# Kernel tuning notes

Measured on AMD Instinct MI355X. Metric: run time of the kernel, lower is better.

## Reference

```python
import jax, jax.numpy as jnp
import numpy as np

N_NODES = 50000
N_EDGES = 800000
F_IN = 256
HIDDEN = 64
HEADS = 4
N_CLASS = 40
NEG_SLOPE = 0.2


def gat_layer(x, src, dst, W, al, ar, b, heads, out_dim):
    # x: [N, Fin] -> h: [N, H, D]
    N = x.shape[0]
    h = (x @ W).reshape(N, heads, out_dim)
    el = jnp.sum(h * al, axis=-1)  # [N, H]
    er = jnp.sum(h * ar, axis=-1)  # [N, H]
    e = jax.nn.leaky_relu(el[src] + er[dst], NEG_SLOPE)  # [E, H]
    # segment softmax over incoming edges of each destination node
    emax = jax.ops.segment_max(e, dst, num_segments=N)  # [N, H] (-inf for empty, unused)
    ex = jnp.exp(e - emax[dst])
    esum = jax.ops.segment_sum(ex, dst, num_segments=N)
    alpha = ex / esum[dst]  # [E, H]; esum[dst] >= ex > 0 per existing edge
    msg = h[src] * alpha[:, :, None]  # [E, H, D]
    out = jax.ops.segment_sum(msg, dst, num_segments=N)  # [N, H, D]
    return out + b.reshape(1, heads, out_dim)


def setup_inputs() -> dict:
    key = jax.random.key(0)
    ks = jax.random.split(key, 16)
    x = jax.random.normal(ks[0], (N_NODES, F_IN), dtype=jnp.float32)
    edge_index = jax.random.randint(ks[1], (2, N_EDGES), 0, N_NODES, dtype=jnp.int64)
    s = 0.1
    return {
        "x": x,
        "edge_index": edge_index,
        "W1": jax.random.normal(ks[2], (F_IN, HEADS * HIDDEN), dtype=jnp.float32) * s,
        "al1": jax.random.normal(ks[3], (HEADS, HIDDEN), dtype=jnp.float32) * s,
        "ar1": jax.random.normal(ks[4], (HEADS, HIDDEN), dtype=jnp.float32) * s,
        "b1": jnp.zeros((HEADS * HIDDEN,), dtype=jnp.float32),
        "W2": jax.random.normal(ks[5], (HEADS * HIDDEN, HEADS * HIDDEN), dtype=jnp.float32) * s,
        "al2": jax.random.normal(ks[6], (HEADS, HIDDEN), dtype=jnp.float32) * s,
        "ar2": jax.random.normal(ks[7], (HEADS, HIDDEN), dtype=jnp.float32) * s,
        "b2": jnp.zeros((HEADS * HIDDEN,), dtype=jnp.float32),
        "W3": jax.random.normal(ks[8], (HEADS * HIDDEN, N_CLASS), dtype=jnp.float32) * s,
        "al3": jax.random.normal(ks[9], (1, N_CLASS), dtype=jnp.float32) * s,
        "ar3": jax.random.normal(ks[10], (1, N_CLASS), dtype=jnp.float32) * s,
        "b3": jnp.zeros((N_CLASS,), dtype=jnp.float32),
    }


def reference(x, edge_index, W1, al1, ar1, b1, W2, al2, ar2, b2, W3, al3, ar3, b3):
    src, dst = edge_index[0], edge_index[1]
    N = x.shape[0]
    # layer 1: GATConv -> flatten heads -> ELU
    h = gat_layer(x, src, dst, W1, al1, ar1, b1, HEADS, HIDDEN).reshape(N, -1)
    h = jax.nn.elu(h)
    # layer 2
    h = gat_layer(h, src, dst, W2, al2, ar2, b2, HEADS, HIDDEN).reshape(N, -1)
    h = jax.nn.elu(h)
    # layer 3: 1 head -> mean over head dim
    h = gat_layer(h, src, dst, W3, al3, ar3, b3, 1, N_CLASS).mean(axis=1)
    return jax.nn.log_softmax(h, axis=1)
```

## Files before the change

kernel.cpp:

```cpp
#include <hip/hip_runtime.h>
#include <hip/hip_bf16.h>
#include <math.h>

#define N_NODES 50000
#define N_EDGES 800000
#define NCLASS 40
#define MAXE 512

using f32x4 = __attribute__((ext_vector_type(4))) float;
using s16x8 = __attribute__((ext_vector_type(8))) short;

__global__ void detect_i64(const int* __restrict__ raw, int* __restrict__ flag) {
  int t = threadIdx.x;
  int v = raw[2 * t + 1];
  unsigned long long any = __ballot(v != 0);
  if (t == 0) flag[0] = (any == 0ULL) ? 1 : 0;
}

__global__ void norm_count(const int* __restrict__ raw, const int* __restrict__ flag,
                           int* __restrict__ s32, int* __restrict__ d32,
                           int* __restrict__ deg) {
  int e = blockIdx.x * blockDim.x + threadIdx.x;
  if (e >= N_EDGES) return;
  int s, d;
  if (flag[0]) {
    s = raw[2 * e];
    d = raw[2 * N_EDGES + 2 * e];
  } else {
    s = raw[e];
    d = raw[N_EDGES + e];
  }
  s32[e] = s;
  d32[e] = d;
  atomicAdd(&deg[d], 1);
}

__global__ void scan_bsum(const int* __restrict__ deg, int* __restrict__ bsums) {
  __shared__ int sm[256];
  int t = threadIdx.x;
  int i = blockIdx.x * 256 + t;
  sm[t] = (i < N_NODES) ? deg[i] : 0;
  __syncthreads();
  for (int off = 128; off > 0; off >>= 1) {
    if (t < off) sm[t] += sm[t + off];
    __syncthreads();
  }
  if (t == 0) bsums[blockIdx.x] = sm[0];
}

__global__ void scan_offsets(int* __restrict__ bsums, int* __restrict__ rowp, int nb) {
  __shared__ int sm[256];
  int t = threadIdx.x;
  int v = (t < nb) ? bsums[t] : 0;
  sm[t] = v;
  __syncthreads();
  for (int off = 1; off < 256; off <<= 1) {
    int add = (t >= off) ? sm[t - off] : 0;
    __syncthreads();
    sm[t] += add;
    __syncthreads();
  }
  if (t < nb) bsums[t] = sm[t] - v;
  if (t == 0) rowp[N_NODES] = N_EDGES;
}

__global__ void scan_final(const int* __restrict__ deg, const int* __restrict__ bsums,
                           int* __restrict__ rowp, int* __restrict__ cursor) {
  __shared__ int sm[256];
  int t = threadIdx.x;
  int i = blockIdx.x * 256 + t;
  int v = (i < N_NODES) ? deg[i] : 0;
  sm[t] = v;
  __syncthreads();
  for (int off = 1; off < 256; off <<= 1) {
    int add = (t >= off) ? sm[t - off] : 0;
    __syncthreads();
    sm[t] += add;
    __syncthreads();
  }
  int excl = sm[t] - v + bsums[blockIdx.x];
  if (i < N_NODES) { rowp[i] = excl; cursor[i] = excl; }
}

__global__ void scatter_edges(const int* __restrict__ s32, const int* __restrict__ d32,
                              int* __restrict__ cursor, int* __restrict__ srcs) {
  int e = blockIdx.x * blockDim.x + threadIdx.x;
  if (e >= N_EDGES) return;
  int d = d32[e];
  int pos = atomicAdd(&cursor[d], 1);
  srcs[pos] = s32[e];
}

__global__ void tr_w(const float* __restrict__ W, __hip_bfloat16* __restrict__ WT) {
  int id = blockIdx.x * 256 + threadIdx.x;
  int n = id >> 8, k = id & 255;
  WT[n * 256 + k] = __float2bfloat16(W[k * 256 + n]);
}

__global__ void tr_w3(const float* __restrict__ W3, __hip_bfloat16* __restrict__ WT3) {
  int id = blockIdx.x * 256 + threadIdx.x;
  int n = id >> 8, k = id & 255;
  WT3[n * 256 + k] = (n < NCLASS) ? __float2bfloat16(W3[k * NCLASS + n]) : __float2bfloat16(0.f);
}

__global__ void cast_x(const float* __restrict__ x, __hip_bfloat16* __restrict__ xb) {
  int id = blockIdx.x * 256 + threadIdx.x;
  float4 v = *reinterpret_cast<const float4*>(x + (size_t)id * 4);
  ushort4 u;
  __hip_bfloat16 b;
  b = __float2bfloat16(v.x); u.x = *(unsigned short*)&b;
  b = __float2bfloat16(v.y); u.y = *(unsigned short*)&b;
  b = __float2bfloat16(v.z); u.z = *(unsigned short*)&b;
  b = __float2bfloat16(v.w); u.w = *(unsigned short*)&b;
  *reinterpret_cast<ushort4*>((unsigned short*)xb + (size_t)id * 4) = u;
}

__global__ __launch_bounds__(256) void gemm_gat12(const __hip_bfloat16* __restrict__ A,
                                                  const __hip_bfloat16* __restrict__ WT,
                                                  const float* __restrict__ al,
                                                  const float* __restrict__ ar,
                                                  __hip_bfloat16* __restrict__ hb,
                                                  float* __restrict__ el,
                                                  float* __restrict__ er) {
  constexpr int MREP = 4, NREP = 4;
  __shared__ __align__(16) __hip_bfloat16 As[128][40];
  __shared__ __align__(16) __hip_bfloat16 Bs[128][40];

  int t = threadIdx.x;
  int lane = t & 63, wave = t >> 6;
  int wr = wave >> 1, wc = wave & 1;
  int row0 = blockIdx.x * 128, col0 = blockIdx.y * 128;
  int ln = lane & 15;
  int kc8 = (lane >> 4) * 8;

  f32x4 acc[MREP][NREP];
  const f32x4 fz = {0.f, 0.f, 0.f, 0.f};
#pragma unroll
  for (int m = 0; m < MREP; ++m)
#pragma unroll
    for (int n = 0; n < NREP; ++n) acc[m][n] = fz;

  for (int k0 = 0; k0 < 256; k0 += 32) {
#pragma unroll
    for (int it = 0; it < 2; ++it) {
      int c = t + it * 256;
      int r = c >> 2, kc = (c & 3) * 8;
      int grow = row0 + r;
      f32x4 v = fz;
      if (grow < N_NODES)
        v = *reinterpret_cast<const f32x4*>(A + (size_t)grow * 256 + k0 + kc);
      *reinterpret_cast<f32x4*>(&As[r][kc]) = v;
    }
#pragma unroll
    for (int it = 0; it < 2; ++it) {
      int c = t + it * 256;
      int r = c >> 2, kc = (c & 3) * 8;
      f32x4 v = *reinterpret_cast<const f32x4*>(WT + (size_t)(col0 + r) * 256 + k0 + kc);
      *reinterpret_cast<f32x4*>(&Bs[r][kc]) = v;
    }
    __syncthreads();
    s16x8 af[MREP], bfr[NREP];
#pragma unroll
    for (int m = 0; m < MREP; ++m)
      af[m] = *reinterpret_cast<const s16x8*>(&As[wr * 64 + m * 16 + ln][kc8]);
#pragma unroll
    for (int n = 0; n < NREP; ++n)
      bfr[n] = *reinterpret_cast<const s16x8*>(&Bs[wc * 64 + n * 16 + ln][kc8]);
#pragma unroll
    for (int m = 0; m < MREP; ++m)
#pragma unroll
      for (int n = 0; n < NREP; ++n)
        acc[m][n] = __builtin_amdgcn_mfma_f32_16x16x32_bf16(af[m], bfr[n], acc[m][n], 0, 0, 0);
    __syncthreads();
  }

  int head = blockIdx.y * 2 + wc;
  float alv[NREP], arv[NREP];
#pragma unroll
  for (int n = 0; n < NREP; ++n) {
    int c = head * 64 + n * 16 + ln;
    alv[n] = al[c];
    arv[n] = ar[c];
  }
#pragma unroll
  for (int m = 0; m < MREP; ++m) {
#pragma unroll
    for (int r = 0; r < 4; ++r) {
      int row = row0 + wr * 64 + m * 16 + (lane >> 4) * 4 + r;
      bool ok = row < N_NODES;
      float pl = 0.f, pr = 0.f;
#pragma unroll
      for (int n = 0; n < NREP; ++n) {
        float v = acc[m][n][r];
        pl += v * alv[n];
        pr += v * arv[n];
        if (ok) hb[(size_t)row * 256 + head * 64 + n * 16 + ln] = __float2bfloat16(v);
      }
      for (int off = 1; off < 16; off <<= 1) {
        pl += __shfl_xor(pl, off);
        pr += __shfl_xor(pr, off);
      }
      if (ln == 0 && ok) {
        el[row * 4 + head] = pl;
        er[row * 4 + head] = pr;
      }
    }
  }
}

__global__ __launch_bounds__(256) void gemm_gat3(const __hip_bfloat16* __restrict__ A,
                                                 const __hip_bfloat16* __restrict__ WT,
                                                 const float* __restrict__ al,
                                                 const float* __restrict__ ar,
                                                 __hip_bfloat16* __restrict__ h3b,
                                                 float* __restrict__ el3,
                                                 float* __restrict__ er3) {
  constexpr int MREP = 2, NREP = 4;
  __shared__ __align__(16) __hip_bfloat16 As[128][40];
  __shared__ __align__(16) __hip_bfloat16 Bs[64][40];

  int t = threadIdx.x;
  int lane = t & 63, wave = t >> 6;
  int row0 = blockIdx.x * 128;
  int ln = lane & 15;
  int kc8 = (lane >> 4) * 8;

  f32x4 acc[MREP][NREP];
  const f32x4 fz = {0.f, 0.f, 0.f, 0.f};
#pragma unroll
  for (int m = 0; m < MREP; ++m)
#pragma unroll
    for (int n = 0; n < NREP; ++n) acc[m][n] = fz;

  for (int k0 = 0; k0 < 256; k0 += 32) {
#pragma unroll
    for (int it = 0; it < 2; ++it) {
      int c = t + it * 256;
      int r = c >> 2, kc = (c & 3) * 8;
      int grow = row0 + r;
      f32x4 v = fz;
      if (grow < N_NODES)
        v = *reinterpret_cast<const f32x4*>(A + (size_t)grow * 256 + k0 + kc);
      *reinterpret_cast<f32x4*>(&As[r][kc]) = v;
    }
    {
      int c = t;
      int r = c >> 2, kc = (c & 3) * 8;
      f32x4 v = *reinterpret_cast<const f32x4*>(WT + (size_t)r * 256 + k0 + kc);
      *reinterpret_cast<f32x4*>(&Bs[r][kc]) = v;
    }
    __syncthreads();
    s16x8 af[MREP], bfr[NREP];
#pragma unroll
    for (int m = 0; m < MREP; ++m)
      af[m] = *reinterpret_cast<const s16x8*>(&As[wave * 32 + m * 16 + ln][kc8]);
#pragma unroll
    for (int n = 0; n < NREP; ++n)
      bfr[n] = *reinterpret_cast<const s16x8*>(&Bs[n * 16 + ln][kc8]);
#pragma unroll
    for (int m = 0; m < MREP; ++m)
#pragma unroll
      for (int n = 0; n < NREP; ++n)
        acc[m][n] = __builtin_amdgcn_mfma_f32_16x16x32_bf16(af[m], bfr[n], acc[m][n], 0, 0, 0);
    __syncthreads();
  }

  float alv[NREP], arv[NREP];
#pragma unroll
  for (int n = 0; n < NREP; ++n) {
    int c = n * 16 + ln;
    alv[n] = (c < NCLASS) ? al[c] : 0.f;
    arv[n] = (c < NCLASS) ? ar[c] : 0.f;
  }
#pragma unroll
  for (int m = 0; m < MREP; ++m) {
#pragma unroll
    for (int r = 0; r < 4; ++r) {
      int row = row0 + wave * 32 + m * 16 + (lane >> 4) * 4 + r;
      bool ok = row < N_NODES;
      float pl = 0.f, pr = 0.f;
#pragma unroll
      for (int n = 0; n < NREP; ++n) {
        float v = acc[m][n][r];
        pl += v * alv[n];
        pr += v * arv[n];
        if (ok) h3b[(size_t)row * 64 + n * 16 + ln] = __float2bfloat16(v);
      }
      for (int off = 1; off < 16; off <<= 1) {
        pl += __shfl_xor(pl, off);
        pr += __shfl_xor(pr, off);
      }
      if (ln == 0 && ok) {
        el3[row] = pl;
        er3[row] = pr;
      }
    }
  }
}

__global__ __launch_bounds__(128) void agg_fused(const __hip_bfloat16* __restrict__ hb,
                                                 const float* __restrict__ el,
                                                 const float* __restrict__ er,
                                                 const float* __restrict__ bias,
                                                 const int* __restrict__ rowp,
                                                 const int* __restrict__ srcs,
                                                 __hip_bfloat16* __restrict__ ob) {
  __shared__ float eld[MAXE * 5];
  __shared__ float mi[8];
  int n = blockIdx.x, t = threadIdx.x;
  int head = t >> 5, slot = t & 31;
  int i0 = rowp[n], deg = rowp[n + 1] - i0;
  float ern = er[n * 4 + head];
  float m = -1e30f, l = 0.f;
  for (int j = slot; j < deg; j += 32) {
    int s = srcs[i0 + j];
    float e = el[s * 4 + head] + ern;
    e = (e >= 0.f) ? e : 0.2f * e;
    if (j < MAXE) eld[j * 5 + head] = e;
    float nm = fmaxf(m, e);
    l = l * __expf(m - nm) + __expf(e - nm);
    m = nm;
  }
  for (int off = 1; off < 32; off <<= 1) {
    float mo = __shfl_xor(m, off), lo = __shfl_xor(l, off);
    float nm = fmaxf(m, mo);
    l = l * __expf(m - nm) + lo * __expf(mo - nm);
    m = nm;
  }
  float inv = (l > 0.f) ? (1.f / l) : 0.f;
  if (slot == 0) { mi[head] = m; mi[4 + head] = inv; }
  __syncthreads();
  int ecount = (deg < MAXE) ? deg : MAXE;
  for (int k = t; k < ecount * 4; k += 128) {
    int j = k >> 2, hh = k & 3;
    eld[j * 5 + hh] = __expf(eld[j * 5 + hh] - mi[hh]) * mi[4 + hh];
  }
  __syncthreads();
  const unsigned int* hp = (const unsigned int*)hb;
  float ax0 = 0.f, ax1 = 0.f, ax2 = 0.f, ax3 = 0.f;
  float ay0 = 0.f, ay1 = 0.f, ay2 = 0.f, ay3 = 0.f;
  int j = 0;
  for (; j + 3 < deg; j += 4) {
    int s0 = srcs[i0 + j], s1 = srcs[i0 + j + 1], s2 = srcs[i0 + j + 2], s3 = srcs[i0 + j + 3];
    float w0, w1, w2, w3;
    if (j + 3 < MAXE) {
      w0 = eld[(j + 0) * 5 + head];
      w1 = eld[(j + 1) * 5 + head];
      w2 = eld[(j + 2) * 5 + head];
      w3 = eld[(j + 3) * 5 + head];
    } else {
      float e0 = el[s0 * 4 + head] + ern; e0 = (e0 >= 0.f) ? e0 : 0.2f * e0;
      float e1 = el[s1 * 4 + head] + ern; e1 = (e1 >= 0.f) ? e1 : 0.2f * e1;
      float e2 = el[s2 * 4 + head] + ern; e2 = (e2 >= 0.f) ? e2 : 0.2f * e2;
      float e3 = el[s3 * 4 + head] + ern; e3 = (e3 >= 0.f) ? e3 : 0.2f * e3;
      w0 = __expf(e0 - m) * inv;
      w1 = __expf(e1 - m) * inv;
      w2 = __expf(e2 - m) * inv;
      w3 = __expf(e3 - m) * inv;
    }
    unsigned int h0 = hp[(size_t)s0 * 128 + t];
    unsigned int h1 = hp[(size_t)s1 * 128 + t];
    unsigned int h2 = hp[(size_t)s2 * 128 + t];
    unsigned int h3v = hp[(size_t)s3 * 128 + t];
    ax0 += w0 * __uint_as_float(h0 << 16);
    ay0 += w0 * __uint_as_float(h0 & 0xffff0000u);
    ax1 += w1 * __uint_as_float(h1 << 16);
    ay1 += w1 * __uint_as_float(h1 & 0xffff0000u);
    ax2 += w2 * __uint_as_float(h2 << 16);
    ay2 += w2 * __uint_as_float(h2 & 0xffff0000u);
    ax3 += w3 * __uint_as_float(h3v << 16);
    ay3 += w3 * __uint_as_float(h3v & 0xffff0000u);
  }
  for (; j < deg; ++j) {
    int s0 = srcs[i0 + j];
    float w0;
    if (j < MAXE) {
      w0 = eld[j * 5 + head];
    } else {
      float e0 = el[s0 * 4 + head] + ern; e0 = (e0 >= 0.f) ? e0 : 0.2f * e0;
      w0 = __expf(e0 - m) * inv;
    }
    unsigned int h0 = hp[(size_t)s0 * 128 + t];
    ax0 += w0 * __uint_as_float(h0 << 16);
    ay0 += w0 * __uint_as_float(h0 & 0xffff0000u);
  }
  float v0 = (ax0 + ax1) + (ax2 + ax3) + bias[2 * t];
  float v1 = (ay0 + ay1) + (ay2 + ay3) + bias[2 * t + 1];
  v0 = (v0 > 0.f) ? v0 : (__expf(v0) - 1.f);
  v1 = (v1 > 0.f) ? v1 : (__expf(v1) - 1.f);
  __hip_bfloat16 b0 = __float2bfloat16(v0), b1 = __float2bfloat16(v1);
  unsigned int packed = (unsigned int)(*(unsigned short*)&b0) |
                        ((unsigned int)(*(unsigned short*)&b1) << 16);
  ((unsigned int*)ob)[(size_t)n * 128 + t] = packed;
}

__global__ __launch_bounds__(64) void agg_cls_fused(const __hip_bfloat16* __restrict__ h3b,
                                                    const float* __restrict__ el3,
                                                    const float* __restrict__ er3,
                                                    const float* __restrict__ bias,
                                                    const int* __restrict__ rowp,
                                                    const int* __restrict__ srcs,
                                                    float* __restrict__ out) {
  __shared__ float eldc[MAXE];
  int n = blockIdx.x, t = threadIdx.x;
  int i0 = rowp[n], deg = rowp[n + 1] - i0;
  float ern = er3[n];
  float m = -1e30f, l = 0.f;
  for (int j = t; j < deg; j += 64) {
    int s = srcs[i0 + j];
    float e = el3[s] + ern;
    e = (e >= 0.f) ? e : 0.2f * e;
    if (j < MAXE) eldc[j] = e;
    float nm = fmaxf(m, e);
    l = l * __expf(m - nm) + __expf(e - nm);
    m = nm;
  }
  for (int off = 1; off < 64; off <<= 1) {
    float mo = __shfl_xor(m, off), lo = __shfl_xor(l, off);
    float nm = fmaxf(m, mo);
    l = l * __expf(m - nm) + lo * __expf(mo - nm);
    m = nm;
  }
  float inv = (l > 0.f) ? (1.f / l) : 0.f;
  __syncthreads();
  int ecount = (deg < MAXE) ? deg : MAXE;
  for (int k = t; k < ecount; k += 64) eldc[k] = __expf(eldc[k] - m) * inv;
  __syncthreads();
  bool act2 = t < ((NCLASS + 1) / 2);
  const unsigned int* hp3 = (const unsigned int*)h3b;
  float ax = 0.f, ay = 0.f, bx = 0.f, by = 0.f;
  int j = 0;
  for (; j + 1 < deg; j += 2) {
    int s0 = srcs[i0 + j], s1 = srcs[i0 + j + 1];
    float w0, w1;
    if (j + 1 < MAXE) {
      w0 = eldc[j];
      w1 = eldc[j + 1];
    } else {
      float e0 = el3[s0] + ern; e0 = (e0 >= 0.f) ? e0 : 0.2f * e0;
      float e1 = el3[s1] + ern; e1 = (e1 >= 0.f) ? e1 : 0.2f * e1;
      w0 = __expf(e0 - m) * inv;
      w1 = __expf(e1 - m) * inv;
    }
    if (act2) {
      unsigned int h0 = hp3[(size_t)s0 * 32 + t];
      unsigned int h1 = hp3[(size_t)s1 * 32 + t];
      ax += w0 * __uint_as_float(h0 << 16);
      ay += w0 * __uint_as_float(h0 & 0xffff0000u);
      bx += w1 * __uint_as_float(h1 << 16);
      by += w1 * __uint_as_float(h1 & 0xffff0000u);
    }
  }
  if (j < deg) {
    int s0 = srcs[i0 + j];
    float w0;
    if (j < MAXE) {
      w0 = eldc[j];
    } else {
      float e0 = el3[s0] + ern; e0 = (e0 >= 0.f) ? e0 : 0.2f * e0;
      w0 = __expf(e0 - m) * inv;
    }
    if (act2) {
      unsigned int h0 = hp3[(size_t)s0 * 32 + t];
      ax += w0 * __uint_as_float(h0 << 16);
      ay += w0 * __uint_as_float(h0 & 0xffff0000u);
    }
  }
  float z0 = ax + bx + (act2 ? bias[2 * t] : 0.f);
  float z1 = ay + by + (act2 ? bias[2 * t + 1] : 0.f);
  float mx = act2 ? fmaxf(z0, z1) : -1e30f;
  for (int off = 32; off > 0; off >>= 1) mx = fmaxf(mx, __shfl_xor(mx, off));
  float sm = act2 ? (__expf(z0 - mx) + __expf(z1 - mx)) : 0.f;
  for (int off = 32; off > 0; off >>= 1) sm += __shfl_xor(sm, off);
  float ls = __logf(sm);
  if (act2) {
    float2 r;
    r.x = z0 - mx - ls;
    r.y = z1 - mx - ls;
    *reinterpret_cast<float2*>(out + (size_t)n * NCLASS + 2 * t) = r;
  }
}

extern "C" void kernel_launch(void* const* d_in, const int* in_sizes, int n_in,
                              void* d_out, int out_size, void* d_ws, size_t ws_size,
                              hipStream_t stream) {
  const float* x   = (const float*)d_in[0];
  const int* edges = (const int*)d_in[1];
  const float* W1  = (const float*)d_in[2];
  const float* al1 = (const float*)d_in[3];
  const float* ar1 = (const float*)d_in[4];
  const float* b1  = (const float*)d_in[5];
  const float* W2  = (const float*)d_in[6];
  const float* al2 = (const float*)d_in[7];
  const float* ar2 = (const float*)d_in[8];
  const float* b2  = (const float*)d_in[9];
  const float* W3  = (const float*)d_in[10];
  const float* al3 = (const float*)d_in[11];
  const float* ar3 = (const float*)d_in[12];
  const float* b3  = (const float*)d_in[13];
  float* out = (float*)d_out;

  const size_t N = N_NODES, E = N_EDGES;
  float* el  = (float*)d_ws;
  float* er  = el + N * 4;
  float* el3 = er + N * 4;
  float* er3 = el3 + N;
  __hip_bfloat16* xb = (__hip_bfloat16*)(er3 + N);
  __hip_bfloat16* hb = xb + N * 256;
  __hip_bfloat16* ob = hb + N * 256;
  __hip_bfloat16* h3b = ob + N * 256;
  __hip_bfloat16* WT = h3b + N * 64;
  __hip_bfloat16* WT3 = WT + 256 * 256;
  int* rowp   = (int*)(WT3 + 64 * 256);
  int* cursor = rowp + (N + 1);
  int* srcs   = cursor + N;
  int* deg    = srcs + E;
  int* bsums  = deg + N;
  int* s32    = bsums + 256;
  int* d32    = s32 + E;
  int* flag   = d32 + E;

  hipMemsetAsync(deg, 0, N * sizeof(int), stream);
  detect_i64<<<1, 64, 0, stream>>>(edges, flag);
  int eb = (int)((E + 255) / 256);
  norm_count<<<eb, 256, 0, stream>>>(edges, flag, s32, d32, deg);
  int nb = (int)((N + 255) / 256);
  scan_bsum<<<nb, 256, 0, stream>>>(deg, bsums);
  scan_offsets<<<1, 256, 0, stream>>>(bsums, rowp, nb);
  scan_final<<<nb, 256, 0, stream>>>(deg, bsums, rowp, cursor);
  scatter_edges<<<eb, 256, 0, stream>>>(s32, d32, cursor, srcs);

  dim3 gg((unsigned)((N + 127) / 128), 2);
  dim3 g3((unsigned)((N + 127) / 128), 1);

  cast_x<<<(unsigned)(N * 256 / 4 / 256), 256, 0, stream>>>(x, xb);
  tr_w<<<256, 256, 0, stream>>>(W1, WT);
  gemm_gat12<<<gg, 256, 0, stream>>>(xb, WT, al1, ar1, hb, el, er);
  agg_fused<<<(unsigned)N, 128, 0, stream>>>(hb, el, er, b1, rowp, srcs, ob);
  tr_w<<<256, 256, 0, stream>>>(W2, WT);
  gemm_gat12<<<gg, 256, 0, stream>>>(ob, WT, al2, ar2, hb, el, er);
  agg_fused<<<(unsigned)N, 128, 0, stream>>>(hb, el, er, b2, rowp, srcs, ob);
  tr_w3<<<64, 256, 0, stream>>>(W3, WT3);
  gemm_gat3<<<g3, 256, 0, stream>>>(ob, WT3, al3, ar3, h3b, el3, er3);
  agg_cls_fused<<<(unsigned)N, 64, 0, stream>>>(h3b, el3, er3, b3, rowp, srcs, out);
}
```

Measured before the change: 474.3 us.

## Map one wavefront per node in aggregation, read raw edges directly, merge weight prep

New measurement: 487.0 us. 1.03x slower.

```diff
diff --git a/kernel.cpp b/kernel.cpp
--- a/kernel.cpp
+++ b/kernel.cpp
@@ -5,7 +5,7 @@
 #define N_NODES 50000
 #define N_EDGES 800000
 #define NCLASS 40
-#define MAXE 512
+#define MAXE 64
 
 using f32x4 = __attribute__((ext_vector_type(4))) float;
 using s16x8 = __attribute__((ext_vector_type(8))) short;
@@ -17,21 +17,11 @@
   if (t == 0) flag[0] = (any == 0ULL) ? 1 : 0;
 }
 
-__global__ void norm_count(const int* __restrict__ raw, const int* __restrict__ flag,
-                           int* __restrict__ s32, int* __restrict__ d32,
-                           int* __restrict__ deg) {
+__global__ void count_raw(const int* __restrict__ raw, const int* __restrict__ flag,
+                          int* __restrict__ deg) {
   int e = blockIdx.x * blockDim.x + threadIdx.x;
   if (e >= N_EDGES) return;
-  int s, d;
-  if (flag[0]) {
-    s = raw[2 * e];
-    d = raw[2 * N_EDGES + 2 * e];
-  } else {
-    s = raw[e];
-    d = raw[N_EDGES + e];
-  }
-  s32[e] = s;
-  d32[e] = d;
+  int d = flag[0] ? raw[2 * N_EDGES + 2 * e] : raw[N_EDGES + e];
   atomicAdd(&deg[d], 1);
 }
 
@@ -82,25 +72,35 @@
   if (i < N_NODES) { rowp[i] = excl; cursor[i] = excl; }
 }
 
-__global__ void scatter_edges(const int* __restrict__ s32, const int* __restrict__ d32,
-                              int* __restrict__ cursor, int* __restrict__ srcs) {
+__global__ void scatter_raw(const int* __restrict__ raw, const int* __restrict__ flag,
+                            int* __restrict__ cursor, int* __restrict__ srcs) {
   int e = blockIdx.x * blockDim.x + threadIdx.x;
   if (e >= N_EDGES) return;
-  int d = d32[e];
+  int f = flag[0];
+  int s = f ? raw[2 * e] : raw[e];
+  int d = f ? raw[2 * N_EDGES + 2 * e] : raw[N_EDGES + e];
   int pos = atomicAdd(&cursor[d], 1);
-  srcs[pos] = s32[e];
-}
-
-__global__ void tr_w(const float* __restrict__ W, __hip_bfloat16* __restrict__ WT) {
-  int id = blockIdx.x * 256 + threadIdx.x;
-  int n = id >> 8, k = id & 255;
-  WT[n * 256 + k] = __float2bfloat16(W[k * 256 + n]);
-}
-
-__global__ void tr_w3(const float* __restrict__ W3, __hip_bfloat16* __restrict__ WT3) {
-  int id = blockIdx.x * 256 + threadIdx.x;
-  int n = id >> 8, k = id & 255;
-  WT3[n * 256 + k] = (n < NCLASS) ? __float2bfloat16(W3[k * NCLASS + n]) : __float2bfloat16(0.f);
+  srcs[pos] = s;
+}
+
+__global__ void prep_w(const float* __restrict__ W1, const float* __restrict__ W2,
+                       const float* __restrict__ W3,
+                       __hip_bfloat16* __restrict__ WT1, __hip_bfloat16* __restrict__ WT2,
+                       __hip_bfloat16* __restrict__ WT3) {
+  int b = blockIdx.x, t = threadIdx.x;
+  if (b < 256) {
+    int id = b * 256 + t;
+    int n = id >> 8, k = id & 255;
+    WT1[n * 256 + k] = __float2bfloat16(W1[k * 256 + n]);
+  } else if (b < 512) {
+    int id = (b - 256) * 256 + t;
+    int n = id >> 8, k = id & 255;
+    WT2[n * 256 + k] = __float2bfloat16(W2[k * 256 + n]);
+  } else {
+    int id = (b - 512) * 256 + t;
+    int n = id >> 8, k = id & 255;
+    WT3[n * 256 + k] = (n < NCLASS) ? __float2bfloat16(W3[k * NCLASS + n]) : __float2bfloat16(0.f);
+  }
 }
 
 __global__ void cast_x(const float* __restrict__ x, __hip_bfloat16* __restrict__ xb) {
@@ -305,116 +305,159 @@
                                                  const int* __restrict__ rowp,
                                                  const int* __restrict__ srcs,
                                                  __hip_bfloat16* __restrict__ ob) {
-  __shared__ float eld[MAXE * 5];
-  __shared__ float mi[8];
-  int n = blockIdx.x, t = threadIdx.x;
-  int head = t >> 5, slot = t & 31;
+  __shared__ float eld[2][MAXE * 4];
+  int wv = threadIdx.x >> 6, lane = threadIdx.x & 63;
+  int n = blockIdx.x * 2 + wv;
+  float* ew = eld[wv];
   int i0 = rowp[n], deg = rowp[n + 1] - i0;
-  float ern = er[n * 4 + head];
-  float m = -1e30f, l = 0.f;
-  for (int j = slot; j < deg; j += 32) {
+  float4 ern4 = *reinterpret_cast<const float4*>(er + (size_t)n * 4);
+  float m0 = -1e30f, m1 = -1e30f, m2 = -1e30f, m3 = -1e30f;
+  float l0 = 0.f, l1 = 0.f, l2 = 0.f, l3 = 0.f;
+  for (int j = lane; j < deg; j += 64) {
     int s = srcs[i0 + j];
-    float e = el[s * 4 + head] + ern;
-    e = (e >= 0.f) ? e : 0.2f * e;
-    if (j < MAXE) eld[j * 5 + head] = e;
-    float nm = fmaxf(m, e);
-    l = l * __expf(m - nm) + __expf(e - nm);
-    m = nm;
-  }
-  for (int off = 1; off < 32; off <<= 1) {
-    float mo = __shfl_xor(m, off), lo = __shfl_xor(l, off);
-    float nm = fmaxf(m, mo);
-    l = l * __expf(m - nm) + lo * __expf(mo - nm);
-    m = nm;
-  }
-  float inv = (l > 0.f) ? (1.f / l) : 0.f;
-  if (slot == 0) { mi[head] = m; mi[4 + head] = inv; }
-  __syncthreads();
-  int ecount = (deg < MAXE) ? deg : MAXE;
-  for (int k = t; k < ecount * 4; k += 128) {
-    int j = k >> 2, hh = k & 3;
-    eld[j * 5 + hh] = __expf(eld[j * 5 + hh] - mi[hh]) * mi[4 + hh];
-  }
-  __syncthreads();
-  const unsigned int* hp = (const unsigned int*)hb;
-  float ax0 = 0.f, ax1 = 0.f, ax2 = 0.f, ax3 = 0.f;
-  float ay0 = 0.f, ay1 = 0.f, ay2 = 0.f, ay3 = 0.f;
+    float4 e4 = *reinterpret_cast<const float4*>(el + (size_t)s * 4);
+    float e0 = e4.x + ern4.x; e0 = (e0 >= 0.f) ? e0 : 0.2f * e0;
+    float e1 = e4.y + ern4.y; e1 = (e1 >= 0.f) ? e1 : 0.2f * e1;
+    float e2 = e4.z + ern4.z; e2 = (e2 >= 0.f) ? e2 : 0.2f * e2;
+    float e3 = e4.w + ern4.w; e3 = (e3 >= 0.f) ? e3 : 0.2f * e3;
+    if (j < MAXE)
+      *reinterpret_cast<float4*>(&ew[j * 4]) = make_float4(e0, e1, e2, e3);
+    float nm;
+    nm = fmaxf(m0, e0); l0 = l0 * __expf(m0 - nm) + __expf(e0 - nm); m0 = nm;
+    nm = fmaxf(m1, e1); l1 = l1 * __expf(m1 - nm) + __expf(e1 - nm); m1 = nm;
+    nm = fmaxf(m2, e2); l2 = l2 * __expf(m2 - nm) + __expf(e2 - nm); m2 = nm;
+    nm = fmaxf(m3, e3); l3 = l3 * __expf(m3 - nm) + __expf(e3 - nm); m3 = nm;
+  }
+#pragma unroll
+  for (int off = 1; off < 64; off <<= 1) {
+    float mo, lo, nm;
+    mo = __shfl_xor(m0, off); lo = __shfl_xor(l0, off);
+    nm = fmaxf(m0, mo); l0 = l0 * __expf(m0 - nm) + lo * __expf(mo - nm); m0 = nm;
+    mo = __shfl_xor(m1, off); lo = __shfl_xor(l1, off);
+    nm = fmaxf(m1, mo); l1 = l1 * __expf(m1 - nm) + lo * __expf(mo - nm); m1 = nm;
+    mo = __shfl_xor(m2, off); lo = __shfl_xor(l2, off);
+    nm = fmaxf(m2, mo); l2 = l2 * __expf(m2 - nm) + lo * __expf(mo - nm); m2 = nm;
+    mo = __shfl_xor(m3, off); lo = __shfl_xor(l3, off);
+    nm = fmaxf(m3, mo); l3 = l3 * __expf(m3 - nm) + lo * __expf(mo - nm); m3 = nm;
+  }
+  float inv0 = (l0 > 0.f) ? (1.f / l0) : 0.f;
+  float inv1 = (l1 > 0.f) ? (1.f / l1) : 0.f;
+  float inv2 = (l2 > 0.f) ? (1.f / l2) : 0.f;
+  float inv3 = (l3 > 0.f) ? (1.f / l3) : 0.f;
+  __syncthreads();
+  int ecount = ((deg < MAXE) ? deg : MAXE) * 4;
+  {
+    int hh = lane & 3;
+    float mm = (hh == 0) ? m0 : (hh == 1) ? m1 : (hh == 2) ? m2 : m3;
+    float iv = (hh == 0) ? inv0 : (hh == 1) ? inv1 : (hh == 2) ? inv2 : inv3;
+    for (int k = lane; k < ecount; k += 64) ew[k] = __expf(ew[k] - mm) * iv;
+  }
+  __syncthreads();
+  int head = lane >> 4;
+  float mh = (head == 0) ? m0 : (head == 1) ? m1 : (head == 2) ? m2 : m3;
+  float ivh = (head == 0) ? inv0 : (head == 1) ? inv1 : (head == 2) ? inv2 : inv3;
+  float ernh = (head == 0) ? ern4.x : (head == 1) ? ern4.y : (head == 2) ? ern4.z : ern4.w;
+  const uint2* hp = (const uint2*)hb;
+  float4 A = make_float4(0.f, 0.f, 0.f, 0.f);
+  float4 B = make_float4(0.f, 0.f, 0.f, 0.f);
+  float4 C = make_float4(0.f, 0.f, 0.f, 0.f);
+  float4 D = make_float4(0.f, 0.f, 0.f, 0.f);
   int j = 0;
   for (; j + 3 < deg; j += 4) {
     int s0 = srcs[i0 + j], s1 = srcs[i0 + j + 1], s2 = srcs[i0 + j + 2], s3 = srcs[i0 + j + 3];
     float w0, w1, w2, w3;
     if (j + 3 < MAXE) {
-      w0 = eld[(j + 0) * 5 + head];
-      w1 = eld[(j + 1) * 5 + head];
-      w2 = eld[(j + 2) * 5 + head];
-      w3 = eld[(j + 3) * 5 + head];
+      w0 = ew[(j + 0) * 4 + head];
+      w1 = ew[(j + 1) * 4 + head];
+      w2 = ew[(j + 2) * 4 + head];
+      w3 = ew[(j + 3) * 4 + head];
     } else {
-      float e0 = el[s0 * 4 + head] + ern; e0 = (e0 >= 0.f) ? e0 : 0.2f * e0;
-      float e1 = el[s1 * 4 + head] + ern; e1 = (e1 >= 0.f) ? e1 : 0.2f * e1;
-      float e2 = el[s2 * 4 + head] + ern; e2 = (e2 >= 0.f) ? e2 : 0.2f * e2;
-      float e3 = el[s3 * 4 + head] + ern; e3 = (e3 >= 0.f) ? e3 : 0.2f * e3;
-      w0 = __expf(e0 - m) * inv;
-      w1 = __expf(e1 - m) * inv;
-      w2 = __expf(e2 - m) * inv;
-      w3 = __expf(e3 - m) * inv;
-    }
-    unsigned int h0 = hp[(size_t)s0 * 128 + t];
-    unsigned int h1 = hp[(size_t)s1 * 128 + t];
-    unsigned int h2 = hp[(size_t)s2 * 128 + t];
-    unsigned int h3v = hp[(size_t)s3 * 128 + t];
-    ax0 += w0 * __uint_as_float(h0 << 16);
-    ay0 += w0 * __uint_as_float(h0 & 0xffff0000u);
-    ax1 += w1 * __uint_as_float(h1 << 16);
-    ay1 += w1 * __uint_as_float(h1 & 0xffff0000u);
-    ax2 += w2 * __uint_as_float(h2 << 16);
-    ay2 += w2 * __uint_as_float(h2 & 0xffff0000u);
-    ax3 += w3 * __uint_as_float(h3v << 16);
-    ay3 += w3 * __uint_as_float(h3v & 0xffff0000u);
+      float e0 = el[s0 * 4 + head] + ernh; e0 = (e0 >= 0.f) ? e0 : 0.2f * e0;
+      float e1 = el[s1 * 4 + head] + ernh; e1 = (e1 >= 0.f) ? e1 : 0.2f * e1;
+      float e2 = el[s2 * 4 + head] + ernh; e2 = (e2 >= 0.f) ? e2 : 0.2f * e2;
+      float e3 = el[s3 * 4 + head] + ernh; e3 = (e3 >= 0.f) ? e3 : 0.2f * e3;
+      w0 = __expf(e0 - mh) * ivh;
+      w1 = __expf(e1 - mh) * ivh;
+      w2 = __expf(e2 - mh) * ivh;
+      w3 = __expf(e3 - mh) * ivh;
+    }
+    uint2 h0 = hp[(size_t)s0 * 64 + lane];
+    uint2 h1 = hp[(size_t)s1 * 64 + lane];
+    uint2 h2 = hp[(size_t)s2 * 64 + lane];
+    uint2 h3v = hp[(size_t)s3 * 64 + lane];
+    A.x += w0 * __uint_as_float(h0.x << 16);
+    A.y += w0 * __uint_as_float(h0.x & 0xffff0000u);
+    A.z += w0 * __uint_as_float(h0.y << 16);
+    A.w += w0 * __uint_as_float(h0.y & 0xffff0000u);
+    B.x += w1 * __uint_as_float(h1.x << 16);
+    B.y += w1 * __uint_as_float(h1.x & 0xffff0000u);
+    B.z += w1 * __uint_as_float(h1.y << 16);
+    B.w += w1 * __uint_as_float(h1.y & 0xffff0000u);
+    C.x += w2 * __uint_as_float(h2.x << 16);
+    C.y += w2 * __uint_as_float(h2.x & 0xffff0000u);
+    C.z += w2 * __uint_as_float(h2.y << 16);
+    C.w += w2 * __uint_as_float(h2.y & 0xffff0000u);
+    D.x += w3 * __uint_as_float(h3v.x << 16);
+    D.y += w3 * __uint_as_float(h3v.x & 0xffff0000u);
+    D.z += w3 * __uint_as_float(h3v.y << 16);
+    D.w += w3 * __uint_as_float(h3v.y & 0xffff0000u);
   }
   for (; j < deg; ++j) {
     int s0 = srcs[i0 + j];
     float w0;
     if (j < MAXE) {
-      w0 = eld[j * 5 + head];
+      w0 = ew[j * 4 + head];
     } else {
-      float e0 = el[s0 * 4 + head] + ern; e0 = (e0 >= 0.f) ? e0 : 0.2f * e0;
-      w0 = __expf(e0 - m) * inv;
-    }
-    unsigned int h0 = hp[(size_t)s0 * 128 + t];
-    ax0 += w0 * __uint_as_float(h0 << 16);
-    ay0 += w0 * __uint_as_float(h0 & 0xffff0000u);
-  }
-  float v0 = (ax0 + ax1) + (ax2 + ax3) + bias[2 * t];
-  float v1 = (ay0 + ay1) + (ay2 + ay3) + bias[2 * t + 1];
-  v0 = (v0 > 0.f) ? v0 : (__expf(v0) - 1.f);
-  v1 = (v1 > 0.f) ? v1 : (__expf(v1) - 1.f);
-  __hip_bfloat16 b0 = __float2bfloat16(v0), b1 = __float2bfloat16(v1);
-  unsigned int packed = (unsigned int)(*(unsigned short*)&b0) |
-                        ((unsigned int)(*(unsigned short*)&b1) << 16);
-  ((unsigned int*)ob)[(size_t)n * 128 + t] = packed;
-}
-
-__global__ __launch_bounds__(64) void agg_cls_fused(const __hip_bfloat16* __restrict__ h3b,
-                                                    const float* __restrict__ el3,
-                                                    const float* __restrict__ er3,
-                                                    const float* __restrict__ bias,
-                                                    const int* __restrict__ rowp,
-                                                    const int* __restrict__ srcs,
-                                                    float* __restrict__ out) {
-  __shared__ float eldc[MAXE];
-  int n = blockIdx.x, t = threadIdx.x;
+      float e0 = el[s0 * 4 + head] + ernh; e0 = (e0 >= 0.f) ? e0 : 0.2f * e0;
+      w0 = __expf(e0 - mh) * ivh;
+    }
+    uint2 h0 = hp[(size_t)s0 * 64 + lane];
+    A.x += w0 * __uint_as_float(h0.x << 16);
+    A.y += w0 * __uint_as_float(h0.x & 0xffff0000u);
+    A.z += w0 * __uint_as_float(h0.y << 16);
+    A.w += w0 * __uint_as_float(h0.y & 0xffff0000u);
+  }
+  float4 b4 = *reinterpret_cast<const float4*>(bias + (size_t)lane * 4);
+  float r0 = (A.x + B.x) + (C.x + D.x) + b4.x;
+  float r1 = (A.y + B.y) + (C.y + D.y) + b4.y;
+  float r2 = (A.z + B.z) + (C.z + D.z) + b4.z;
+  float r3 = (A.w + B.w) + (C.w + D.w) + b4.w;
+  r0 = (r0 > 0.f) ? r0 : (__expf(r0) - 1.f);
+  r1 = (r1 > 0.f) ? r1 : (__expf(r1) - 1.f);
+  r2 = (r2 > 0.f) ? r2 : (__expf(r2) - 1.f);
+  r3 = (r3 > 0.f) ? r3 : (__expf(r3) - 1.f);
+  __hip_bfloat16 q0 = __float2bfloat16(r0), q1 = __float2bfloat16(r1);
+  __hip_bfloat16 q2 = __float2bfloat16(r2), q3 = __float2bfloat16(r3);
+  uint2 o;
+  o.x = (unsigned int)(*(unsigned short*)&q0) | ((unsigned int)(*(unsigned short*)&q1) << 16);
+  o.y = (unsigned int)(*(unsigned short*)&q2) | ((unsigned int)(*(unsigned short*)&q3) << 16);
+  ((uint2*)ob)[(size_t)n * 64 + lane] = o;
+}
+
+__global__ __launch_bounds__(128) void agg_cls_fused(const __hip_bfloat16* __restrict__ h3b,
+                                                     const float* __restrict__ el3,
+                                                     const float* __restrict__ er3,
+                                                     const float* __restrict__ bias,
+                                                     const int* __restrict__ rowp,
+                                                     const int* __restrict__ srcs,
+                                                     float* __restrict__ out) {
+  __shared__ float eldc[2][MAXE];
+  int wv = threadIdx.x >> 6, lane = threadIdx.x & 63;
+  int n = blockIdx.x * 2 + wv;
+  float* ec = eldc[wv];
   int i0 = rowp[n], deg = rowp[n + 1] - i0;
   float ern = er3[n];
   float m = -1e30f, l = 0.f;
-  for (int j = t; j < deg; j += 64) {
+  for (int j = lane; j < deg; j += 64) {
     int s = srcs[i0 + j];
     float e = el3[s] + ern;
     e = (e >= 0.f) ? e : 0.2f * e;
-    if (j < MAXE) eldc[j] = e;
+    if (j < MAXE) ec[j] = e;
     float nm = fmaxf(m, e);
     l = l * __expf(m - nm) + __expf(e - nm);
     m = nm;
   }
+#pragma unroll
   for (int off = 1; off < 64; off <<= 1) {
     float mo = __shfl_xor(m, off), lo = __shfl_xor(l, off);
     float nm = fmaxf(m, mo);
@@ -424,9 +467,9 @@
   float inv = (l > 0.f) ? (1.f / l) : 0.f;
   __syncthreads();
   int ecount = (deg < MAXE) ? deg : MAXE;
-  for (int k = t; k < ecount; k += 64) eldc[k] = __expf(eldc[k] - m) * inv;
-  __syncthreads();
-  bool act2 = t < ((NCLASS + 1) / 2);
+  for (int k = lane; k < ecount; k += 64) ec[k] = __expf(ec[k] - m) * inv;
+  __syncthreads();
+  bool act2 = lane < ((NCLASS + 1) / 2);
   const unsigned int* hp3 = (const unsigned int*)h3b;
   float ax = 0.f, ay = 0.f, bx = 0.f, by = 0.f;
   int j = 0;
@@ -434,8 +477,8 @@
     int s0 = srcs[i0 + j], s1 = srcs[i0 + j + 1];
     float w0, w1;
     if (j + 1 < MAXE) {
-      w0 = eldc[j];
-      w1 = eldc[j + 1];
+      w0 = ec[j];
+      w1 = ec[j + 1];
     } else {
       float e0 = el3[s0] + ern; e0 = (e0 >= 0.f) ? e0 : 0.2f * e0;
       float e1 = el3[s1] + ern; e1 = (e1 >= 0.f) ? e1 : 0.2f * e1;
@@ -443,8 +486,8 @@
       w1 = __expf(e1 - m) * inv;
     }
     if (act2) {
-      unsigned int h0 = hp3[(size_t)s0 * 32 + t];
-      unsigned int h1 = hp3[(size_t)s1 * 32 + t];
+      unsigned int h0 = hp3[(size_t)s0 * 32 + lane];
+      unsigned int h1 = hp3[(size_t)s1 * 32 + lane];
       ax += w0 * __uint_as_float(h0 << 16);
       ay += w0 * __uint_as_float(h0 & 0xffff0000u);
       bx += w1 * __uint_as_float(h1 << 16);
@@ -455,19 +498,19 @@
     int s0 = srcs[i0 + j];
     float w0;
     if (j < MAXE) {
-      w0 = eldc[j];
+      w0 = ec[j];
     } else {
       float e0 = el3[s0] + ern; e0 = (e0 >= 0.f) ? e0 : 0.2f * e0;
       w0 = __expf(e0 - m) * inv;
     }
     if (act2) {
-      unsigned int h0 = hp3[(size_t)s0 * 32 + t];
+      unsigned int h0 = hp3[(size_t)s0 * 32 + lane];
       ax += w0 * __uint_as_float(h0 << 16);
       ay += w0 * __uint_as_float(h0 & 0xffff0000u);
     }
   }
-  float z0 = ax + bx + (act2 ? bias[2 * t] : 0.f);
-  float z1 = ay + by + (act2 ? bias[2 * t + 1] : 0.f);
+  float z0 = ax + bx + (act2 ? bias[2 * lane] : 0.f);
+  float z1 = ay + by + (act2 ? bias[2 * lane + 1] : 0.f);
   float mx = act2 ? fmaxf(z0, z1) : -1e30f;
   for (int off = 32; off > 0; off >>= 1) mx = fmaxf(mx, __shfl_xor(mx, off));
   float sm = act2 ? (__expf(z0 - mx) + __expf(z1 - mx)) : 0.f;
@@ -477,7 +520,7 @@
     float2 r;
     r.x = z0 - mx - ls;
     r.y = z1 - mx - ls;
-    *reinterpret_cast<float2*>(out + (size_t)n * NCLASS + 2 * t) = r;
+    *reinterpret_cast<float2*>(out + (size_t)n * NCLASS + 2 * lane) = r;
   }
 }
 
@@ -509,38 +552,36 @@
   __hip_bfloat16* hb = xb + N * 256;
   __hip_bfloat16* ob = hb + N * 256;
   __hip_bfloat16* h3b = ob + N * 256;
-  __hip_bfloat16* WT = h3b + N * 64;
-  __hip_bfloat16* WT3 = WT + 256 * 256;
+  __hip_bfloat16* WT1 = h3b + N * 64;
+  __hip_bfloat16* WT2 = WT1 + 256 * 256;
+  __hip_bfloat16* WT3 = WT2 + 256 * 256;
   int* rowp   = (int*)(WT3 + 64 * 256);
   int* cursor = rowp + (N + 1);
   int* srcs   = cursor + N;
   int* deg    = srcs + E;
   int* bsums  = deg + N;
-  int* s32    = bsums + 256;
-  int* d32    = s32 + E;
-  int* flag   = d32 + E;
+  int* flag   = bsums + 256;
 
   hipMemsetAsync(deg, 0, N * sizeof(int), stream);
   detect_i64<<<1, 64, 0, stream>>>(edges, flag);
   int eb = (int)((E + 255) / 256);
-  norm_count<<<eb, 256, 0, stream>>>(edges, flag, s32, d32, deg);
+  count_raw<<<eb, 256, 0, stream>>>(edges, flag, deg);
   int nb = (int)((N + 255) / 256);
   scan_bsum<<<nb, 256, 0, stream>>>(deg, bsums);
   scan_offsets<<<1, 256, 0, stream>>>(bsums, rowp, nb);
   scan_final<<<nb, 256, 0, stream>>>(deg, bsums, rowp, cursor);
-  scatter_edges<<<eb, 256, 0, stream>>>(s32, d32, cursor, srcs);
+  scatter_raw<<<eb, 256, 0, stream>>>(edges, flag, cursor, srcs);
+
+  cast_x<<<(unsigned)(N * 256 / 4 / 256), 256, 0, stream>>>(x, xb);
+  prep_w<<<576, 256, 0, stream>>>(W1, W2, W3, WT1, WT2, WT3);
 
   dim3 gg((unsigned)((N + 127) / 128), 2);
   dim3 g3((unsigned)((N + 127) / 128), 1);
 
-  cast_x<<<(unsigned)(N * 256 / 4 / 256), 256, 0, stream>>>(x, xb);
-  tr_w<<<256, 256, 0, stream>>>(W1, WT);
-  gemm_gat12<<<gg, 256, 0, stream>>>(xb, WT, al1, ar1, hb, el, er);
-  agg_fused<<<(unsigned)N, 128, 0, stream>>>(hb, el, er, b1, rowp, srcs, ob);
-  tr_w<<<256, 256, 0, stream>>>(W2, WT);
-  gemm_gat12<<<gg, 256, 0, stream>>>(ob, WT, al2, ar2, hb, el, er);
-  agg_fused<<<(unsigned)N, 128, 0, stream>>>(hb, el, er, b2, rowp, srcs, ob);
-  tr_w3<<<64, 256, 0, stream>>>(W3, WT3);
+  gemm_gat12<<<gg, 256, 0, stream>>>(xb, WT1, al1, ar1, hb, el, er);
+  agg_fused<<<(unsigned)(N / 2), 128, 0, stream>>>(hb, el, er, b1, rowp, srcs, ob);
+  gemm_gat12<<<gg, 256, 0, stream>>>(ob, WT2, al2, ar2, hb, el, er);
+  agg_fused<<<(unsigned)(N / 2), 128, 0, stream>>>(hb, el, er, b2, rowp, srcs, ob);
   gemm_gat3<<<g3, 256, 0, stream>>>(ob, WT3, al3, ar3, h3b, el3, er3);
-  agg_cls_fused<<<(unsigned)N, 64, 0, stream>>>(h3b, el3, er3, b3, rowp, srcs, out);
-}
+  agg_cls_fused<<<(unsigned)(N / 2), 128, 0, stream>>>(h3b, el3, er3, b3, rowp, srcs, out);
+}
```
